# Performance work log

Hardware: AMD Instinct MI355X
Metric: run time of the kernel (lower is better)

The kernel has to match this reference:

```python
import jax, jax.numpy as jnp
import numpy as np

DIM = 512
HEADS = 8
SEQ = 2048
BATCH = 4


def setup_inputs() -> dict:
    key = jax.random.key(0)
    k = jax.random.split(key, 6)
    x = jax.random.normal(k[0], (BATCH, SEQ, DIM), dtype=jnp.float32)
    mask = jax.random.normal(k[1], (BATCH, SEQ, SEQ), dtype=jnp.float32)
    Wqkv = jax.random.normal(k[2], (3 * DIM, DIM), dtype=jnp.float32) * 0.02
    Btab = jax.random.normal(k[3], (1, HEADS, 2 * SEQ - 1), dtype=jnp.float32) * 0.02
    Wproj = jax.random.normal(k[4], (DIM, DIM), dtype=jnp.float32) * 0.02
    bproj = jax.random.normal(k[5], (DIM,), dtype=jnp.float32) * 0.02
    return {"x": x, "mask": mask, "Wqkv": Wqkv, "Btab": Btab,
            "Wproj": Wproj, "bproj": bproj}


def reference(x, mask, Wqkv, Btab, Wproj, bproj):
    B, N, C = x.shape
    H = Btab.shape[1]
    seq = (Btab.shape[2] + 1) // 2
    head_dim = C // H
    scale = head_dim ** (-0.5)

    # qkv projection (no bias), split into q,k,v of shape [B,H,N,head_dim]
    qkv = (x @ Wqkv.T).reshape(B, N, 3, H, head_dim)
    qkv = jnp.transpose(qkv, (2, 0, 3, 1, 4))  # [3,B,H,N,hd]
    q, k, v = qkv[0], qkv[1], qkv[2]

    # gathered relative-position bias: B_index[i,j] = i - j + seq - 1
    idx = jnp.arange(N)[:, None] - jnp.arange(N)[None, :] + (seq - 1)  # [N,N]
    bias = Btab[:, :, idx]  # [1,H,N,N]

    attn = jnp.einsum('bhnd,bhmd->bhnm', q, k) * scale + bias
    attn = attn + mask[:, None, :, :]  # additive mask, broadcast over heads
    attn = jax.nn.softmax(attn, axis=-1)

    out = jnp.einsum('bhnm,bhmd->bhnd', attn, v)  # [B,H,N,hd]
    out = jnp.transpose(out, (0, 2, 1, 3)).reshape(B, N, C)
    return out @ Wproj.T + bproj
```

## Files before the change

kernel.cpp:

```cpp
#include <hip/hip_runtime.h>


typedef __attribute__((ext_vector_type(8))) short short8;
typedef __attribute__((ext_vector_type(4))) float f32x4;

#define SEQ   2048
#define NHEAD 8
#define NBATCH 4
#define HD    64
#define CDIM  512

__device__ __forceinline__ unsigned short f32_to_bf16_rn(float f) {
  unsigned u = __builtin_bit_cast(unsigned, f);
  u += 0x7FFFu + ((u >> 16) & 1u);
  return (unsigned short)(u >> 16);
}

__global__ __launch_bounds__(256) void cvt_f32_bf16(const float* __restrict__ in,
                                                    ushort* __restrict__ out, int n4) {
  int i = blockIdx.x * 256 + threadIdx.x;
  const int stride = gridDim.x * 256;
  for (; i < n4; i += stride) {
    float4 v = reinterpret_cast<const float4*>(in)[i];
    ushort4 o;
    o.x = f32_to_bf16_rn(v.x);
    o.y = f32_to_bf16_rn(v.y);
    o.z = f32_to_bf16_rn(v.z);
    o.w = f32_to_bf16_rn(v.w);
    reinterpret_cast<ushort4*>(out)[i] = o;
  }
}

template <int MODE>
__global__ __launch_bounds__(256) void gemm_nt(
    const ushort* __restrict__ A, const ushort* __restrict__ Bm,
    ushort* __restrict__ qo, ushort* __restrict__ ko, ushort* __restrict__ vto,
    const float* __restrict__ bias, float* __restrict__ outf) {
  const int K = 512;
  __shared__ ushort As[128 * 40];
  __shared__ ushort Bs[128 * 40];

  const int t = threadIdx.x;
  const int bn = blockIdx.x, bm = blockIdx.y;
  const int lane = t & 63, w = t >> 6;
  const int wm = w >> 1, wn = w & 1;
  const int lr = lane & 15, lq = lane >> 4;
  const int m0 = bm * 128, n0 = bn * 128;

  f32x4 acc[4][4];
#pragma unroll
  for (int i = 0; i < 4; ++i)
#pragma unroll
    for (int j = 0; j < 4; ++j) acc[i][j] = (f32x4){0.f, 0.f, 0.f, 0.f};

  for (int kt = 0; kt < K; kt += 32) {
#pragma unroll
    for (int p = 0; p < 2; ++p) {
      const int flat = p * 256 + t;
      const int row = flat >> 2, seg = flat & 3;
      *(uint4*)&As[row * 40 + seg * 8] =
          *(const uint4*)(A + (size_t)(m0 + row) * K + kt + seg * 8);
      *(uint4*)&Bs[row * 40 + seg * 8] =
          *(const uint4*)(Bm + (size_t)(n0 + row) * K + kt + seg * 8);
    }
    __syncthreads();

    short8 af[4], bf[4];
#pragma unroll
    for (int i = 0; i < 4; ++i) {
      af[i] = *(const short8*)&As[(wm * 64 + i * 16 + lr) * 40 + lq * 8];
      bf[i] = *(const short8*)&Bs[(wn * 64 + i * 16 + lr) * 40 + lq * 8];
    }
#pragma unroll
    for (int i = 0; i < 4; ++i)
#pragma unroll
      for (int j = 0; j < 4; ++j)
        acc[i][j] = __builtin_amdgcn_mfma_f32_16x16x32_bf16(af[i], bf[j], acc[i][j], 0, 0, 0);
    __syncthreads();
  }

  if constexpr (MODE == 0) {
#pragma unroll
    for (int i = 0; i < 4; ++i) {
      const int mbase = m0 + wm * 64 + i * 16 + lq * 4;
      const int bb = mbase >> 11;
      const int s0 = mbase & 2047;
#pragma unroll
      for (int j = 0; j < 4; ++j) {
        const int nb = n0 + wn * 64 + j * 16;
        const int tt = nb >> 9;
        const int hh = (nb >> 6) & 7;
        const int d0 = nb & 63;
        const int bh = bb * NHEAD + hh;
        if (tt == 2) {
          ushort4 pk;
          pk.x = f32_to_bf16_rn(acc[i][j][0]);
          pk.y = f32_to_bf16_rn(acc[i][j][1]);
          pk.z = f32_to_bf16_rn(acc[i][j][2]);
          pk.w = f32_to_bf16_rn(acc[i][j][3]);
          *(ushort4*)(vto + ((size_t)bh * HD + d0 + lr) * SEQ + s0) = pk;
        } else {
          ushort* dst = (tt == 0) ? qo : ko;
#pragma unroll
          for (int r = 0; r < 4; ++r)
            dst[((size_t)bh * SEQ + s0 + r) * HD + d0 + lr] = f32_to_bf16_rn(acc[i][j][r]);
        }
      }
    }
  } else {
#pragma unroll
    for (int i = 0; i < 4; ++i) {
#pragma unroll
      for (int j = 0; j < 4; ++j) {
        const int n = n0 + wn * 64 + j * 16 + lr;
        const float bv = bias[n];
#pragma unroll
        for (int r = 0; r < 4; ++r) {
          const int m = m0 + wm * 64 + i * 16 + lq * 4 + r;
          outf[(size_t)m * 512 + n] = acc[i][j][r] + bv;
        }
      }
    }
  }
}

__global__ __launch_bounds__(256) void attn_fused(
    const ushort* __restrict__ Q, const ushort* __restrict__ Kt,
    const ushort* __restrict__ VT, const float* __restrict__ mask,
    const float* __restrict__ Btab, ushort* __restrict__ Out) {
  __shared__ ushort Ks[64 * 72];
  __shared__ ushort Vs[64 * 72];
  __shared__ ushort Ps[4][16 * 68];
  __shared__ float Bw[2112];

  const int flat = blockIdx.x;
  const int xcd = flat & 7;
  const int rr = flat >> 3;
  const int h = rr & 7;
  const int slot = rr >> 3;
  const int g = slot * 8 + xcd;
  const int qt = g & 31, b = g >> 5;

  const int bh = b * NHEAD + h;
  const ushort* qh = Q + (size_t)bh * SEQ * HD;
  const ushort* kh = Kt + (size_t)bh * SEQ * HD;
  const ushort* vh = VT + (size_t)bh * HD * SEQ;
  const float* mb = mask + (size_t)b * SEQ * SEQ;
  const float* bt = Btab + h * (2 * SEQ - 1);

  const int t = threadIdx.x;
  const int lane = t & 63, w = t >> 6;
  const int lr = lane & 15, lq = lane >> 4;
  const int qb0 = qt * 64;
  const int qbase = qb0 + w * 16;

  for (int i = t; i < 2111; i += 256) Bw[i] = bt[qb0 + i] * 1.44269504f;

  short8 qf0, qf1;
  {
    const ushort* qp = qh + (size_t)(qbase + lr) * HD + lq * 8;
    qf0 = *(const short8*)qp;
    qf1 = *(const short8*)(qp + 32);
  }

  const float* mrow[4];
#pragma unroll
  for (int r = 0; r < 4; ++r) mrow[r] = mb + (size_t)(qbase + lq * 4 + r) * SEQ + lr;

  float l_r[4] = {0.f, 0.f, 0.f, 0.f};
  f32x4 of[4];
#pragma unroll
  for (int i = 0; i < 4; ++i) of[i] = (f32x4){0.f, 0.f, 0.f, 0.f};

  const int qrl = w * 16 + lq * 4;
  const int srow = t >> 3;
  const int sseg = t & 7;

  float mnext[4][4];
#pragma unroll
  for (int f = 0; f < 4; ++f)
#pragma unroll
    for (int r = 0; r < 4; ++r) mnext[f][r] = mrow[r][f * 16];

  for (int kv0 = 0; kv0 < SEQ; kv0 += 64) {
    float mc[4][4];
#pragma unroll
    for (int f = 0; f < 4; ++f)
#pragma unroll
      for (int r = 0; r < 4; ++r) mc[f][r] = mnext[f][r];
    if (kv0 + 64 < SEQ) {
#pragma unroll
      for (int f = 0; f < 4; ++f)
#pragma unroll
        for (int r = 0; r < 4; ++r) mnext[f][r] = mrow[r][kv0 + 64 + f * 16];
    }

    __syncthreads();
#pragma unroll
    for (int p = 0; p < 2; ++p) {
      const int row = p * 32 + srow;
      *(uint4*)&Ks[row * 72 + sseg * 8] =
          *(const uint4*)(kh + (size_t)(kv0 + row) * HD + sseg * 8);
      *(uint4*)&Vs[row * 72 + sseg * 8] =
          *(const uint4*)(vh + (size_t)row * SEQ + kv0 + sseg * 8);
    }
    __syncthreads();

    f32x4 sf[4];
#pragma unroll
    for (int f = 0; f < 4; ++f) {
      sf[f] = (f32x4){0.f, 0.f, 0.f, 0.f};
      const ushort* kp = &Ks[(f * 16 + lr) * 72 + lq * 8];
      const short8 k0 = *(const short8*)kp;
      const short8 k1 = *(const short8*)(kp + 32);
      sf[f] = __builtin_amdgcn_mfma_f32_16x16x32_bf16(qf0, k0, sf[f], 0, 0, 0);
      sf[f] = __builtin_amdgcn_mfma_f32_16x16x32_bf16(qf1, k1, sf[f], 0, 0, 0);
    }

    float rs[4] = {0.f, 0.f, 0.f, 0.f};
#pragma unroll
    for (int f = 0; f < 4; ++f) {
      const int ib = qrl - (kv0 + f * 16 + lr) + 2047;
#pragma unroll
      for (int r = 0; r < 4; ++r) {
        const float xs = fmaf(sf[f][r], 0.18033688f,
                              fmaf(mc[f][r], 1.44269504f, Bw[ib + r]));
        const float p = __builtin_amdgcn_exp2f(xs);
        rs[r] += p;
        const unsigned u = __builtin_bit_cast(unsigned, p);
        Ps[w][(lq * 4 + r) * 68 + f * 16 + lr] =
            (unsigned short)((u + 0x8000u) >> 16);
      }
    }
#pragma unroll
    for (int r = 0; r < 4; ++r) {
      float v = rs[r];
      v += __shfl_xor(v, 1);
      v += __shfl_xor(v, 2);
      v += __shfl_xor(v, 4);
      v += __shfl_xor(v, 8);
      l_r[r] += v;
    }

#pragma unroll
    for (int ks = 0; ks < 2; ++ks) {
      union { uint2 u[2]; short8 s; } pu;
      const int pidx = lr * 68 + ks * 32 + lq * 8;
      pu.u[0] = *(const uint2*)&Ps[w][pidx];
      pu.u[1] = *(const uint2*)&Ps[w][pidx + 4];
#pragma unroll
      for (int hf = 0; hf < 4; ++hf) {
        const short8 vf = *(const short8*)&Vs[(hf * 16 + lr) * 72 + ks * 32 + lq * 8];
        of[hf] = __builtin_amdgcn_mfma_f32_16x16x32_bf16(pu.s, vf, of[hf], 0, 0, 0);
      }
    }
  }

#pragma unroll
  for (int r = 0; r < 4; ++r) {
    const float inv = 1.0f / l_r[r];
    const int qr = qbase + lq * 4 + r;
    ushort* op = Out + ((size_t)(b * SEQ + qr)) * CDIM + h * HD;
#pragma unroll
    for (int hf = 0; hf < 4; ++hf) op[hf * 16 + lr] = f32_to_bf16_rn(of[hf][r] * inv);
  }
}

extern "C" void kernel_launch(void* const* d_in, const int* in_sizes, int n_in,
                              void* d_out, int out_size, void* d_ws, size_t ws_size,
                              hipStream_t stream) {
  const float* x     = (const float*)d_in[0];
  const float* mask  = (const float*)d_in[1];
  const float* Wqkv  = (const float*)d_in[2];
  const float* Btab  = (const float*)d_in[3];
  const float* Wproj = (const float*)d_in[4];
  const float* bproj = (const float*)d_in[5];
  float* out = (float*)d_out;

  char* ws = (char*)d_ws;
  const size_t SZ_X   = (size_t)NBATCH * SEQ * CDIM;
  const size_t SZ_QKV = (size_t)3 * CDIM * CDIM;
  const size_t SZ_PRJ = (size_t)CDIM * CDIM;
  const size_t SZ_HD  = (size_t)NBATCH * NHEAD * SEQ * HD;

  ushort* xb    = (ushort*)ws; ws += SZ_X * 2;
  ushort* wqkvb = (ushort*)ws; ws += SZ_QKV * 2;
  ushort* wprjb = (ushort*)ws; ws += SZ_PRJ * 2;
  ushort* qb    = (ushort*)ws; ws += SZ_HD * 2;
  ushort* kb    = (ushort*)ws; ws += SZ_HD * 2;
  ushort* vtb   = (ushort*)ws; ws += SZ_HD * 2;
  ushort* aob   = (ushort*)ws; ws += SZ_X * 2;

  {
    int n4 = (int)(SZ_X / 4);
    int g = (n4 + 255) / 256; if (g > 4096) g = 4096;
    cvt_f32_bf16<<<g, 256, 0, stream>>>(x, xb, n4);
  }
  {
    int n4 = (int)(SZ_QKV / 4);
    cvt_f32_bf16<<<(n4 + 255) / 256, 256, 0, stream>>>(Wqkv, wqkvb, n4);
  }
  {
    int n4 = (int)(SZ_PRJ / 4);
    cvt_f32_bf16<<<(n4 + 255) / 256, 256, 0, stream>>>(Wproj, wprjb, n4);
  }

  gemm_nt<0><<<dim3(12, 64), 256, 0, stream>>>(xb, wqkvb, qb, kb, vtb, nullptr, nullptr);

  attn_fused<<<dim3(1024), 256, 0, stream>>>(qb, kb, vtb, mask, Btab, aob);

  gemm_nt<1><<<dim3(4, 64), 256, 0, stream>>>(aob, wprjb, nullptr, nullptr, nullptr, bproj, out);
}
```

Before: 164.3 us.

## Prefetch K/V tiles into registers, store bias table as bf16, raise occupancy

Adds register double-buffering for K/V: the next tile's global loads are issued right after the LDS store, so they overlap the current tile's compute instead of stalling before it. Mask prefetch moves to after the softmax exponentials, and the rel-pos bias table in LDS becomes bf16 to cut shared memory use. The kernel also gets a launch_bounds occupancy hint of 5 and s_setprio around the MFMA sections. In exchange, the bf16 bias loses some precision and the extra registers may conflict with the occupancy target.

```diff
diff --git a/kernel.cpp b/kernel.cpp
--- a/kernel.cpp
+++ b/kernel.cpp
@@ -124,14 +124,14 @@
   }
 }
 
-__global__ __launch_bounds__(256) void attn_fused(
+__global__ __launch_bounds__(256, 5) void attn_fused(
     const ushort* __restrict__ Q, const ushort* __restrict__ Kt,
     const ushort* __restrict__ VT, const float* __restrict__ mask,
     const float* __restrict__ Btab, ushort* __restrict__ Out) {
   __shared__ ushort Ks[64 * 72];
   __shared__ ushort Vs[64 * 72];
   __shared__ ushort Ps[4][16 * 68];
-  __shared__ float Bw[2112];
+  __shared__ ushort Bw[2112];
 
   const int flat = blockIdx.x;
   const int xcd = flat & 7;
@@ -154,7 +154,8 @@
   const int qb0 = qt * 64;
   const int qbase = qb0 + w * 16;
 
-  for (int i = t; i < 2111; i += 256) Bw[i] = bt[qb0 + i] * 1.44269504f;
+  for (int i = t; i < 2111; i += 256)
+    Bw[i] = f32_to_bf16_rn(bt[qb0 + i] * 1.44269504f);
 
   short8 qf0, qf1;
   {
@@ -176,6 +177,13 @@
   const int srow = t >> 3;
   const int sseg = t & 7;
 
+  uint4 kreg[2], vreg[2];
+#pragma unroll
+  for (int p = 0; p < 2; ++p) {
+    const int row = p * 32 + srow;
+    kreg[p] = *(const uint4*)(kh + (size_t)row * HD + sseg * 8);
+    vreg[p] = *(const uint4*)(vh + (size_t)row * SEQ + sseg * 8);
+  }
   float mnext[4][4];
 #pragma unroll
   for (int f = 0; f < 4; ++f)
@@ -183,30 +191,28 @@
     for (int r = 0; r < 4; ++r) mnext[f][r] = mrow[r][f * 16];
 
   for (int kv0 = 0; kv0 < SEQ; kv0 += 64) {
-    float mc[4][4];
-#pragma unroll
-    for (int f = 0; f < 4; ++f)
-#pragma unroll
-      for (int r = 0; r < 4; ++r) mc[f][r] = mnext[f][r];
-    if (kv0 + 64 < SEQ) {
-#pragma unroll
-      for (int f = 0; f < 4; ++f)
-#pragma unroll
-        for (int r = 0; r < 4; ++r) mnext[f][r] = mrow[r][kv0 + 64 + f * 16];
-    }
-
     __syncthreads();
-#pragma unroll
-    for (int p = 0; p < 2; ++p) {
-      const int row = p * 32 + srow;
-      *(uint4*)&Ks[row * 72 + sseg * 8] =
-          *(const uint4*)(kh + (size_t)(kv0 + row) * HD + sseg * 8);
-      *(uint4*)&Vs[row * 72 + sseg * 8] =
-          *(const uint4*)(vh + (size_t)row * SEQ + kv0 + sseg * 8);
+    {
+      const int row0 = srow, row1 = 32 + srow;
+      *(uint4*)&Ks[row0 * 72 + sseg * 8] = kreg[0];
+      *(uint4*)&Vs[row0 * 72 + sseg * 8] = vreg[0];
+      *(uint4*)&Ks[row1 * 72 + sseg * 8] = kreg[1];
+      *(uint4*)&Vs[row1 * 72 + sseg * 8] = vreg[1];
     }
     __syncthreads();
 
+    const int nkv = kv0 + 64;
+    if (nkv < SEQ) {
+#pragma unroll
+      for (int p = 0; p < 2; ++p) {
+        const int row = p * 32 + srow;
+        kreg[p] = *(const uint4*)(kh + (size_t)(nkv + row) * HD + sseg * 8);
+        vreg[p] = *(const uint4*)(vh + (size_t)row * SEQ + nkv + sseg * 8);
+      }
+    }
+
     f32x4 sf[4];
+    __builtin_amdgcn_s_setprio(1);
 #pragma unroll
     for (int f = 0; f < 4; ++f) {
       sf[f] = (f32x4){0.f, 0.f, 0.f, 0.f};
@@ -216,6 +222,7 @@
       sf[f] = __builtin_amdgcn_mfma_f32_16x16x32_bf16(qf0, k0, sf[f], 0, 0, 0);
       sf[f] = __builtin_amdgcn_mfma_f32_16x16x32_bf16(qf1, k1, sf[f], 0, 0, 0);
     }
+    __builtin_amdgcn_s_setprio(0);
 
     float rs[4] = {0.f, 0.f, 0.f, 0.f};
 #pragma unroll
@@ -223,8 +230,9 @@
       const int ib = qrl - (kv0 + f * 16 + lr) + 2047;
 #pragma unroll
       for (int r = 0; r < 4; ++r) {
+        const float bw = __builtin_bit_cast(float, ((unsigned)Bw[ib + r]) << 16);
         const float xs = fmaf(sf[f][r], 0.18033688f,
-                              fmaf(mc[f][r], 1.44269504f, Bw[ib + r]));
+                              fmaf(mnext[f][r], 1.44269504f, bw));
         const float p = __builtin_amdgcn_exp2f(xs);
         rs[r] += p;
         const unsigned u = __builtin_bit_cast(unsigned, p);
@@ -232,6 +240,14 @@
             (unsigned short)((u + 0x8000u) >> 16);
       }
     }
+
+    if (nkv < SEQ) {
+#pragma unroll
+      for (int f = 0; f < 4; ++f)
+#pragma unroll
+        for (int r = 0; r < 4; ++r) mnext[f][r] = mrow[r][nkv + f * 16];
+    }
+
 #pragma unroll
     for (int r = 0; r < 4; ++r) {
       float v = rs[r];
@@ -242,6 +258,7 @@
       l_r[r] += v;
     }
 
+    __builtin_amdgcn_s_setprio(1);
 #pragma unroll
     for (int ks = 0; ks < 2; ++ks) {
       union { uint2 u[2]; short8 s; } pu;
@@ -254,6 +271,7 @@
         of[hf] = __builtin_amdgcn_mfma_f32_16x16x32_bf16(pu.s, vf, of[hf], 0, 0, 0);
       }
     }
+    __builtin_amdgcn_s_setprio(0);
   }
 
 #pragma unroll
```

After: 245.7 us. 1.49x slower.

## Process two 16-row Q sub-tiles per wave and register-prefetch K/V tiles

Applied to the files above, without the earlier changes.

The attention kernel drops from 4 to 2 waves per block, with each wave handling 32 query rows as two 16-row halves that share every K and V fragment read from LDS. The next K/V tile is prefetched into registers while the current one is computed, and mask loads for the second half are staggered. The bias window is stored in LDS as bf16 to halve its footprint, and row sums are reduced across lanes once at the end instead of every tile. In exchange it uses more registers, has fewer waves per block to hide latency, and rounds the bias to bf16.

```diff
diff --git a/kernel.cpp b/kernel.cpp
--- a/kernel.cpp
+++ b/kernel.cpp
@@ -124,14 +124,14 @@
   }
 }
 
-__global__ __launch_bounds__(256) void attn_fused(
+__global__ __launch_bounds__(128) void attn_fused(
     const ushort* __restrict__ Q, const ushort* __restrict__ Kt,
     const ushort* __restrict__ VT, const float* __restrict__ mask,
     const float* __restrict__ Btab, ushort* __restrict__ Out) {
   __shared__ ushort Ks[64 * 72];
   __shared__ ushort Vs[64 * 72];
-  __shared__ ushort Ps[4][16 * 68];
-  __shared__ float Bw[2112];
+  __shared__ ushort Ps[2][32 * 68];
+  __shared__ ushort Bw[2112];
 
   const int flat = blockIdx.x;
   const int xcd = flat & 7;
@@ -152,117 +152,179 @@
   const int lane = t & 63, w = t >> 6;
   const int lr = lane & 15, lq = lane >> 4;
   const int qb0 = qt * 64;
-  const int qbase = qb0 + w * 16;
-
-  for (int i = t; i < 2111; i += 256) Bw[i] = bt[qb0 + i] * 1.44269504f;
-
-  short8 qf0, qf1;
+  const int qbaseA = qb0 + w * 32;
+  const int qbaseB = qbaseA + 16;
+
+  for (int i = t; i < 2111; i += 128)
+    Bw[i] = f32_to_bf16_rn(bt[qb0 + i] * 1.44269504f);
+
+  short8 qfA0, qfA1, qfB0, qfB1;
   {
-    const ushort* qp = qh + (size_t)(qbase + lr) * HD + lq * 8;
-    qf0 = *(const short8*)qp;
-    qf1 = *(const short8*)(qp + 32);
-  }
-
-  const float* mrow[4];
-#pragma unroll
-  for (int r = 0; r < 4; ++r) mrow[r] = mb + (size_t)(qbase + lq * 4 + r) * SEQ + lr;
-
-  float l_r[4] = {0.f, 0.f, 0.f, 0.f};
-  f32x4 of[4];
-#pragma unroll
-  for (int i = 0; i < 4; ++i) of[i] = (f32x4){0.f, 0.f, 0.f, 0.f};
-
-  const int qrl = w * 16 + lq * 4;
+    const ushort* qpA = qh + (size_t)(qbaseA + lr) * HD + lq * 8;
+    qfA0 = *(const short8*)qpA;
+    qfA1 = *(const short8*)(qpA + 32);
+    const ushort* qpB = qh + (size_t)(qbaseB + lr) * HD + lq * 8;
+    qfB0 = *(const short8*)qpB;
+    qfB1 = *(const short8*)(qpB + 32);
+  }
+
+  const float* mpA = mb + (size_t)(qbaseA + lq * 4) * SEQ + lr;
+  const float* mpB = mb + (size_t)(qbaseB + lq * 4) * SEQ + lr;
+
+  float lA0 = 0.f, lA1 = 0.f, lA2 = 0.f, lA3 = 0.f;
+  float lB0 = 0.f, lB1 = 0.f, lB2 = 0.f, lB3 = 0.f;
+  f32x4 ofA[4], ofB[4];
+#pragma unroll
+  for (int i = 0; i < 4; ++i) {
+    ofA[i] = (f32x4){0.f, 0.f, 0.f, 0.f};
+    ofB[i] = (f32x4){0.f, 0.f, 0.f, 0.f};
+  }
+
+  const int qrlA = w * 32 + lq * 4;
   const int srow = t >> 3;
   const int sseg = t & 7;
 
-  float mnext[4][4];
+  const ushort* kp = kh + (size_t)srow * HD + sseg * 8;
+  const ushort* vp = vh + (size_t)srow * SEQ + sseg * 8;
+
+  uint4 kr0 = *(const uint4*)(kp);
+  uint4 kr1 = *(const uint4*)(kp + 1024);
+  uint4 kr2 = *(const uint4*)(kp + 2048);
+  uint4 kr3 = *(const uint4*)(kp + 3072);
+  uint4 vr0 = *(const uint4*)(vp);
+  uint4 vr1 = *(const uint4*)(vp + 16 * SEQ);
+  uint4 vr2 = *(const uint4*)(vp + 32 * SEQ);
+  uint4 vr3 = *(const uint4*)(vp + 48 * SEQ);
+  float mnA[4][4];
 #pragma unroll
   for (int f = 0; f < 4; ++f)
 #pragma unroll
-    for (int r = 0; r < 4; ++r) mnext[f][r] = mrow[r][f * 16];
+    for (int r = 0; r < 4; ++r) mnA[f][r] = mpA[(size_t)r * SEQ + f * 16];
 
   for (int kv0 = 0; kv0 < SEQ; kv0 += 64) {
-    float mc[4][4];
+    __syncthreads();
+    *(uint4*)&Ks[(srow)*72 + sseg * 8] = kr0;
+    *(uint4*)&Ks[(16 + srow) * 72 + sseg * 8] = kr1;
+    *(uint4*)&Ks[(32 + srow) * 72 + sseg * 8] = kr2;
+    *(uint4*)&Ks[(48 + srow) * 72 + sseg * 8] = kr3;
+    *(uint4*)&Vs[(srow)*72 + sseg * 8] = vr0;
+    *(uint4*)&Vs[(16 + srow) * 72 + sseg * 8] = vr1;
+    *(uint4*)&Vs[(32 + srow) * 72 + sseg * 8] = vr2;
+    *(uint4*)&Vs[(48 + srow) * 72 + sseg * 8] = vr3;
+    __syncthreads();
+
+    const int nkv = (kv0 + 64 < SEQ) ? (kv0 + 64) : 0;
+
+    float mnB[4][4];
 #pragma unroll
     for (int f = 0; f < 4; ++f)
 #pragma unroll
-      for (int r = 0; r < 4; ++r) mc[f][r] = mnext[f][r];
-    if (kv0 + 64 < SEQ) {
-#pragma unroll
-      for (int f = 0; f < 4; ++f)
-#pragma unroll
-        for (int r = 0; r < 4; ++r) mnext[f][r] = mrow[r][kv0 + 64 + f * 16];
-    }
-
-    __syncthreads();
-#pragma unroll
-    for (int p = 0; p < 2; ++p) {
-      const int row = p * 32 + srow;
-      *(uint4*)&Ks[row * 72 + sseg * 8] =
-          *(const uint4*)(kh + (size_t)(kv0 + row) * HD + sseg * 8);
-      *(uint4*)&Vs[row * 72 + sseg * 8] =
-          *(const uint4*)(vh + (size_t)row * SEQ + kv0 + sseg * 8);
-    }
-    __syncthreads();
-
-    f32x4 sf[4];
+      for (int r = 0; r < 4; ++r) mnB[f][r] = mpB[(size_t)r * SEQ + kv0 + f * 16];
+
+    f32x4 sfA[4], sfB[4];
 #pragma unroll
     for (int f = 0; f < 4; ++f) {
-      sf[f] = (f32x4){0.f, 0.f, 0.f, 0.f};
-      const ushort* kp = &Ks[(f * 16 + lr) * 72 + lq * 8];
-      const short8 k0 = *(const short8*)kp;
-      const short8 k1 = *(const short8*)(kp + 32);
-      sf[f] = __builtin_amdgcn_mfma_f32_16x16x32_bf16(qf0, k0, sf[f], 0, 0, 0);
-      sf[f] = __builtin_amdgcn_mfma_f32_16x16x32_bf16(qf1, k1, sf[f], 0, 0, 0);
-    }
-
-    float rs[4] = {0.f, 0.f, 0.f, 0.f};
+      const ushort* kfp = &Ks[(f * 16 + lr) * 72 + lq * 8];
+      const short8 k0 = *(const short8*)kfp;
+      const short8 k1 = *(const short8*)(kfp + 32);
+      sfA[f] = (f32x4){0.f, 0.f, 0.f, 0.f};
+      sfA[f] = __builtin_amdgcn_mfma_f32_16x16x32_bf16(qfA0, k0, sfA[f], 0, 0, 0);
+      sfA[f] = __builtin_amdgcn_mfma_f32_16x16x32_bf16(qfA1, k1, sfA[f], 0, 0, 0);
+      sfB[f] = (f32x4){0.f, 0.f, 0.f, 0.f};
+      sfB[f] = __builtin_amdgcn_mfma_f32_16x16x32_bf16(qfB0, k0, sfB[f], 0, 0, 0);
+      sfB[f] = __builtin_amdgcn_mfma_f32_16x16x32_bf16(qfB1, k1, sfB[f], 0, 0, 0);
+    }
+
 #pragma unroll
     for (int f = 0; f < 4; ++f) {
-      const int ib = qrl - (kv0 + f * 16 + lr) + 2047;
+      const int ib = qrlA - (kv0 + f * 16 + lr) + 2047;
 #pragma unroll
       for (int r = 0; r < 4; ++r) {
-        const float xs = fmaf(sf[f][r], 0.18033688f,
-                              fmaf(mc[f][r], 1.44269504f, Bw[ib + r]));
+        const float bw = __builtin_bit_cast(float, ((unsigned)Bw[ib + r]) << 16);
+        const float xs = fmaf(sfA[f][r], 0.18033688f,
+                              fmaf(mnA[f][r], 1.44269504f, bw));
         const float p = __builtin_amdgcn_exp2f(xs);
-        rs[r] += p;
+        if (r == 0) lA0 += p; else if (r == 1) lA1 += p;
+        else if (r == 2) lA2 += p; else lA3 += p;
         const unsigned u = __builtin_bit_cast(unsigned, p);
         Ps[w][(lq * 4 + r) * 68 + f * 16 + lr] =
             (unsigned short)((u + 0x8000u) >> 16);
       }
     }
-#pragma unroll
-    for (int r = 0; r < 4; ++r) {
-      float v = rs[r];
-      v += __shfl_xor(v, 1);
-      v += __shfl_xor(v, 2);
-      v += __shfl_xor(v, 4);
-      v += __shfl_xor(v, 8);
-      l_r[r] += v;
-    }
+
+#pragma unroll
+    for (int f = 0; f < 4; ++f)
+#pragma unroll
+      for (int r = 0; r < 4; ++r) mnA[f][r] = mpA[(size_t)r * SEQ + nkv + f * 16];
+
+#pragma unroll
+    for (int f = 0; f < 4; ++f) {
+      const int ib = qrlA + 16 - (kv0 + f * 16 + lr) + 2047;
+#pragma unroll
+      for (int r = 0; r < 4; ++r) {
+        const float bw = __builtin_bit_cast(float, ((unsigned)Bw[ib + r]) << 16);
+        const float xs = fmaf(sfB[f][r], 0.18033688f,
+                              fmaf(mnB[f][r], 1.44269504f, bw));
+        const float p = __builtin_amdgcn_exp2f(xs);
+        if (r == 0) lB0 += p; else if (r == 1) lB1 += p;
+        else if (r == 2) lB2 += p; else lB3 += p;
+        const unsigned u = __builtin_bit_cast(unsigned, p);
+        Ps[w][(16 + lq * 4 + r) * 68 + f * 16 + lr] =
+            (unsigned short)((u + 0x8000u) >> 16);
+      }
+    }
+
+    kr0 = *(const uint4*)(kp + (size_t)nkv * HD);
+    kr1 = *(const uint4*)(kp + (size_t)nkv * HD + 1024);
+    kr2 = *(const uint4*)(kp + (size_t)nkv * HD + 2048);
+    kr3 = *(const uint4*)(kp + (size_t)nkv * HD + 3072);
+    vr0 = *(const uint4*)(vp + nkv);
+    vr1 = *(const uint4*)(vp + nkv + 16 * SEQ);
+    vr2 = *(const uint4*)(vp + nkv + 32 * SEQ);
+    vr3 = *(const uint4*)(vp + nkv + 48 * SEQ);
 
 #pragma unroll
     for (int ks = 0; ks < 2; ++ks) {
-      union { uint2 u[2]; short8 s; } pu;
-      const int pidx = lr * 68 + ks * 32 + lq * 8;
-      pu.u[0] = *(const uint2*)&Ps[w][pidx];
-      pu.u[1] = *(const uint2*)&Ps[w][pidx + 4];
+      union { uint2 u[2]; short8 s; } puA, puB;
+      const int pbase = ks * 32 + lq * 8;
+      puA.u[0] = *(const uint2*)&Ps[w][lr * 68 + pbase];
+      puA.u[1] = *(const uint2*)&Ps[w][lr * 68 + pbase + 4];
+      puB.u[0] = *(const uint2*)&Ps[w][(16 + lr) * 68 + pbase];
+      puB.u[1] = *(const uint2*)&Ps[w][(16 + lr) * 68 + pbase + 4];
 #pragma unroll
       for (int hf = 0; hf < 4; ++hf) {
         const short8 vf = *(const short8*)&Vs[(hf * 16 + lr) * 72 + ks * 32 + lq * 8];
-        of[hf] = __builtin_amdgcn_mfma_f32_16x16x32_bf16(pu.s, vf, of[hf], 0, 0, 0);
-      }
-    }
-  }
-
+        ofA[hf] = __builtin_amdgcn_mfma_f32_16x16x32_bf16(puA.s, vf, ofA[hf], 0, 0, 0);
+        ofB[hf] = __builtin_amdgcn_mfma_f32_16x16x32_bf16(puB.s, vf, ofB[hf], 0, 0, 0);
+      }
+    }
+  }
+
+  float lA[4] = {lA0, lA1, lA2, lA3};
+  float lB[4] = {lB0, lB1, lB2, lB3};
 #pragma unroll
   for (int r = 0; r < 4; ++r) {
-    const float inv = 1.0f / l_r[r];
-    const int qr = qbase + lq * 4 + r;
-    ushort* op = Out + ((size_t)(b * SEQ + qr)) * CDIM + h * HD;
-#pragma unroll
-    for (int hf = 0; hf < 4; ++hf) op[hf * 16 + lr] = f32_to_bf16_rn(of[hf][r] * inv);
+    float v = lA[r];
+    v += __shfl_xor(v, 1); v += __shfl_xor(v, 2);
+    v += __shfl_xor(v, 4); v += __shfl_xor(v, 8);
+    lA[r] = v;
+    float u = lB[r];
+    u += __shfl_xor(u, 1); u += __shfl_xor(u, 2);
+    u += __shfl_xor(u, 4); u += __shfl_xor(u, 8);
+    lB[r] = u;
+  }
+#pragma unroll
+  for (int r = 0; r < 4; ++r) {
+    const float invA = 1.0f / lA[r];
+    const int qrA = qbaseA + lq * 4 + r;
+    ushort* opA = Out + ((size_t)(b * SEQ + qrA)) * CDIM + h * HD;
+#pragma unroll
+    for (int hf = 0; hf < 4; ++hf) opA[hf * 16 + lr] = f32_to_bf16_rn(ofA[hf][r] * invA);
+    const float invB = 1.0f / lB[r];
+    const int qrB = qbaseB + lq * 4 + r;
+    ushort* opB = Out + ((size_t)(b * SEQ + qrB)) * CDIM + h * HD;
+#pragma unroll
+    for (int hf = 0; hf < 4; ++hf) opB[hf * 16 + lr] = f32_to_bf16_rn(ofB[hf][r] * invB);
   }
 }
 
@@ -307,7 +369,7 @@
 
   gemm_nt<0><<<dim3(12, 64), 256, 0, stream>>>(xb, wqkvb, qb, kb, vtb, nullptr, nullptr);
 
-  attn_fused<<<dim3(1024), 256, 0, stream>>>(qb, kb, vtb, mask, Btab, aob);
+  attn_fused<<<dim3(1024), 128, 0, stream>>>(qb, kb, vtb, mask, Btab, aob);
 
   gemm_nt<1><<<dim3(4, 64), 256, 0, stream>>>(aob, wprjb, nullptr, nullptr, nullptr, bproj, out);
 }
```

After: 142.9 us. -13.0%, faster.
